# Kernel optimization log

Hardware: AMD Instinct MI355X
Metric: run time of the kernel (lower is better)

## Reference

```python
import jax, jax.numpy as jnp
import numpy as np


def _patches3x3(x):
    # x: [B,H,W,C] -> [B,H,W,9,C], SAME zero padding, patch index k = i*3+j
    B, H, W, C = x.shape
    p = jnp.pad(x, ((0, 0), (1, 1), (1, 1), (0, 0)))
    return jnp.stack([p[:, i:i + H, j:j + W, :] for i in range(3) for j in range(3)], axis=3)


def setup_inputs() -> dict:
    key = jax.random.key(0)
    k1, k2, k3 = jax.random.split(key, 3)
    B, H, W, CH, NC, DIM = 4, 80, 80, 256, 22, 256
    x = jax.random.normal(k1, (B, H, W, CH), dtype=jnp.float32)
    seg_mask = jax.random.uniform(k2, (B, H, W, NC), dtype=jnp.float32)
    # he_uniform over receptive field ch*3*3
    lim = np.sqrt(6.0 / (CH * 9)).astype(np.float32)
    conv_w = jax.random.uniform(k3, (CH, 3, 3, DIM), dtype=jnp.float32, minval=-lim, maxval=lim)
    return {"x": x, "seg_mask": seg_mask, "conv_w": conv_w}


def reference(x, seg_mask, conv_w):
    B, H, W, CH = x.shape
    NC = seg_mask.shape[-1]
    DIM = conv_w.shape[-1]
    # patches of segmentation map: [B,H,W,9,NC]
    s_patch = _patches3x3(seg_mask)
    m = seg_mask[:, :, :, None, :]                       # [B,H,W,1,NC]
    s_max = jnp.max(m, axis=-1, keepdims=True)           # [B,H,W,1,1]
    # keep patch values only for the argmax class at the center pixel
    sel = jnp.sum(jnp.where(m == s_max, s_patch, 0.0), axis=-1)  # [B,H,W,9]
    cnt = jnp.sum((sel != 0.0).astype(jnp.float32), axis=-1, keepdims=True)  # [B,H,W,1]
    norm = jnp.where(cnt > 0, 9.0 / jnp.maximum(cnt, 1.0), 0.0)  # divide_no_nan(9, cnt)
    # per-channel 3x3 patch extraction of features (== depthwise conv with eye(9))
    xp = _patches3x3(x)                                  # [B,H,W,9,CH]
    xp = xp * sel[..., None]                             # mask-gated patches
    w = conv_w.reshape(CH, 9, DIM)
    out = jnp.einsum('bhwkc,ckd->bhwd', xp, w) * norm    # [B,H,W,DIM]
    return out
```

## Files before the change

kernel.cpp:

```cpp
#include <hip/hip_runtime.h>
#include <hip/hip_bf16.h>
#include <cstdint>

#define B_ 4
#define H_ 80
#define W_ 80
#define CH_ 256
#define NC_ 22
#define DIM_ 256
#define NPIX (B_*H_*W_)

typedef unsigned short ushort;
typedef __attribute__((ext_vector_type(8))) short short8;
typedef __attribute__((ext_vector_type(4))) float floatx4;

static __device__ inline ushort f2bf(float v) {
    __hip_bfloat16 h = __float2bfloat16(v);
    ushort r;
    __builtin_memcpy(&r, &h, 2);
    return r;
}
static __device__ inline unsigned pk2(float a, float b) {
    return (unsigned)f2bf(a) | ((unsigned)f2bf(b) << 16);
}

static __device__ inline void gll16(const ushort* g, ushort* l) {
    __builtin_amdgcn_global_load_lds(
        (const __attribute__((address_space(1))) unsigned int*)g,
        (__attribute__((address_space(3))) unsigned int*)l, 16, 0, 0);
}

__global__ __launch_bounds__(256) void prep(const float* __restrict__ cw,
                                            const float* __restrict__ x,
                                            ushort* __restrict__ wbT,
                                            ushort* __restrict__ xb)
{
    __shared__ ushort ls[32][260];
    if (blockIdx.x >= 72) {
        const int bid = blockIdx.x - 72;
        const size_t idx = ((size_t)bid * 256 + threadIdx.x) * 8;
        const float4* s = (const float4*)(x + idx);
        float4 a = s[0], b = s[1];
        *(uint4*)(xb + idx) = make_uint4(pk2(a.x, a.y), pk2(a.z, a.w),
                                         pk2(b.x, b.y), pk2(b.z, b.w));
        if (bid == 0 && threadIdx.x < 64)
            *(uint4*)(xb + (size_t)NPIX * CH_ + threadIdx.x * 8) = make_uint4(0, 0, 0, 0);
        return;
    }
    const int k  = blockIdx.x / 8;
    const int c0 = (blockIdx.x % 8) * 32;
    const int c   = threadIdx.x >> 3;
    const int sg  = threadIdx.x & 7;

    const float* src = cw + ((size_t)(c0 + c) * 9 + k) * DIM_ + sg * 32;
    #pragma unroll
    for (int e = 0; e < 32; e += 4) {
        float4 v = *(const float4*)(src + e);
        unsigned* dst = (unsigned*)&ls[c][sg * 32 + e];
        dst[0] = pk2(v.x, v.y);
        dst[1] = pk2(v.z, v.w);
    }
    __syncthreads();

    const int d = threadIdx.x;
    ushort tmp[32];
    #pragma unroll
    for (int cc = 0; cc < 32; ++cc) tmp[cc] = ls[cc][d];
    uint4 o[4];
    __builtin_memcpy(o, tmp, 64);
    uint4* dst = (uint4*)(wbT + ((size_t)k * 256 + d) * 256 + c0);
    dst[0] = o[0]; dst[1] = o[1]; dst[2] = o[2]; dst[3] = o[3];
}

__global__ __launch_bounds__(256, 3) void conv3(const ushort* __restrict__ xb,
                                                const float* __restrict__ seg,
                                                const ushort* __restrict__ wbT,
                                                float* __restrict__ out)
{
    __shared__ ushort xs[2][84 * 128];
    __shared__ float  sl[9][80];

    const int tid  = threadIdx.x;
    const int lane = tid & 63;
    const int wv   = tid >> 6;
    const int ln   = lane & 15;
    const int quad = lane >> 4;
    const int d0   = blockIdx.x * 128;
    const int rt   = blockIdx.y;
    const int b    = rt / H_;
    const int h    = rt % H_;
    const ushort* zpad = xb + (size_t)NPIX * CH_;

    const int rho0 = lane >> 4;
    const int cp   = lane & 15;
    auto stage = [&](int p, int buf) {
        const int i  = p >> 1;
        const int cc = (p & 1) * 128;
        const int r  = h + i - 1;
        const bool rowok = (r >= 0) && (r < H_);
        for (int g = wv; g < 21; g += 4) {
            const int rho = g * 4 + rho0;
            const int scn = (cp & 8) | ((cp ^ rho) & 7);
            const int col = rho - 1;
            const bool v = rowok && (col >= 0) && (col < W_);
            const ushort* src = v ? (xb + (((size_t)(b * H_ + r)) * W_ + col) * CH_
                                        + cc + scn * 8)
                                  : zpad;
            gll16(src, &xs[buf][g * 512]);
        }
    };

    stage(0, 0);

    if (tid < W_) {
        const int m = tid;
        const float2* c2 = (const float2*)(seg + ((size_t)(b * H_ + h) * W_ + m) * NC_);
        float cv[NC_];
        #pragma unroll
        for (int c = 0; c < NC_ / 2; ++c) { float2 v = c2[c]; cv[2*c] = v.x; cv[2*c+1] = v.y; }
        float mx = -1e30f;
        #pragma unroll
        for (int c = 0; c < NC_; ++c) mx = fmaxf(mx, cv[c]);
        float sel[9];
        int cnt = 0;
        #pragma unroll
        for (int k = 0; k < 9; ++k) {
            int i = k / 3, j = k % 3;
            int hh = h + i - 1, ww = m + j - 1;
            float s = 0.f;
            if (hh >= 0 && hh < H_ && ww >= 0 && ww < W_) {
                const float2* n2 = (const float2*)(seg + ((size_t)(b * H_ + hh) * W_ + ww) * NC_);
                #pragma unroll
                for (int c = 0; c < NC_ / 2; ++c) {
                    float2 v = n2[c];
                    s += (cv[2*c]   == mx) ? v.x : 0.f;
                    s += (cv[2*c+1] == mx) ? v.y : 0.f;
                }
            }
            sel[k] = s;
            cnt += (s != 0.f) ? 1 : 0;
        }
        float norm = (cnt > 0) ? 9.f / (float)cnt : 0.f;
        #pragma unroll
        for (int k = 0; k < 9; ++k) sl[k][m] = sel[k] * norm;
    }

    floatx4 O[5][2];
    #pragma unroll
    for (int im = 0; im < 5; ++im)
        #pragma unroll
        for (int jn = 0; jn < 2; ++jn)
            O[im][jn] = (floatx4){0.f, 0.f, 0.f, 0.f};

    __syncthreads();

    for (int p = 0; p < 6; ++p) {
        const int buf = p & 1;
        const int i   = p >> 1;
        const int cc  = (p & 1) * 128;
        if (p < 5) stage(p + 1, buf ^ 1);

        #pragma unroll
        for (int j = 0; j < 3; ++j) {
            const int k = 3 * i + j;

            short8 Breg[8];
            #pragma unroll
            for (int kk = 0; kk < 4; ++kk)
                #pragma unroll
                for (int jn = 0; jn < 2; ++jn)
                    Breg[kk * 2 + jn] = *(const short8*)(wbT
                        + ((size_t)k * 256 + d0 + wv * 32 + jn * 16 + ln) * 256
                        + cc + kk * 32 + quad * 8);

            floatx4 P[5][2];
            #pragma unroll
            for (int im = 0; im < 5; ++im)
                #pragma unroll
                for (int jn = 0; jn < 2; ++jn)
                    P[im][jn] = (floatx4){0.f, 0.f, 0.f, 0.f};

            #pragma unroll
            for (int kk = 0; kk < 4; ++kk) {
                short8 a[5];
                #pragma unroll
                for (int im = 0; im < 5; ++im) {
                    const int rho = im * 16 + ln + j;
                    const int Gc  = 4 * kk + quad;
                    const int ch  = (Gc & 8) | ((Gc ^ rho) & 7);
                    a[im] = *(const short8*)&xs[buf][rho * 128 + ch * 8];
                }
                #pragma unroll
                for (int im = 0; im < 5; ++im)
                    #pragma unroll
                    for (int jn = 0; jn < 2; ++jn)
                        P[im][jn] = __builtin_amdgcn_mfma_f32_16x16x32_bf16(
                            a[im], Breg[kk * 2 + jn], P[im][jn], 0, 0, 0);
            }

            #pragma unroll
            for (int im = 0; im < 5; ++im) {
                const floatx4 sv = *(const floatx4*)&sl[k][im * 16 + quad * 4];
                #pragma unroll
                for (int jn = 0; jn < 2; ++jn) {
                    O[im][jn][0] += sv[0] * P[im][jn][0];
                    O[im][jn][1] += sv[1] * P[im][jn][1];
                    O[im][jn][2] += sv[2] * P[im][jn][2];
                    O[im][jn][3] += sv[3] * P[im][jn][3];
                }
            }
        }
        __syncthreads();
    }

    #pragma unroll
    for (int im = 0; im < 5; ++im) {
        #pragma unroll
        for (int jn = 0; jn < 2; ++jn) {
            const int dd = d0 + wv * 32 + jn * 16 + ln;
            #pragma unroll
            for (int r = 0; r < 4; ++r) {
                const int m = im * 16 + quad * 4 + r;
                out[((size_t)(rt * W_ + m)) * DIM_ + dd] = O[im][jn][r];
            }
        }
    }
}

extern "C" void kernel_launch(void* const* d_in, const int* in_sizes, int n_in,
                              void* d_out, int out_size, void* d_ws, size_t ws_size,
                              hipStream_t stream)
{
    const float* x   = (const float*)d_in[0];
    const float* seg = (const float*)d_in[1];
    const float* cw  = (const float*)d_in[2];
    float* out = (float*)d_out;

    ushort* wbT = (ushort*)d_ws;
    ushort* xb  = (ushort*)((char*)d_ws + 1179648);

    prep<<<dim3(72 + NPIX * CH_ / (256 * 8)), dim3(256), 0, stream>>>(cw, x, wbT, xb);
    conv3<<<dim3(2, B_ * H_), dim3(256), 0, stream>>>(xb, seg, wbT, out);
}
```

Baseline: 177.9 us.

## Fuse fp32-to-bf16 conversion of x into conv kernel staging

```diff
diff --git a/kernel.cpp b/kernel.cpp
--- a/kernel.cpp
+++ b/kernel.cpp
@@ -24,33 +24,14 @@
     return (unsigned)f2bf(a) | ((unsigned)f2bf(b) << 16);
 }
 
-static __device__ inline void gll16(const ushort* g, ushort* l) {
-    __builtin_amdgcn_global_load_lds(
-        (const __attribute__((address_space(1))) unsigned int*)g,
-        (__attribute__((address_space(3))) unsigned int*)l, 16, 0, 0);
-}
-
 __global__ __launch_bounds__(256) void prep(const float* __restrict__ cw,
-                                            const float* __restrict__ x,
-                                            ushort* __restrict__ wbT,
-                                            ushort* __restrict__ xb)
+                                            ushort* __restrict__ wbT)
 {
     __shared__ ushort ls[32][260];
-    if (blockIdx.x >= 72) {
-        const int bid = blockIdx.x - 72;
-        const size_t idx = ((size_t)bid * 256 + threadIdx.x) * 8;
-        const float4* s = (const float4*)(x + idx);
-        float4 a = s[0], b = s[1];
-        *(uint4*)(xb + idx) = make_uint4(pk2(a.x, a.y), pk2(a.z, a.w),
-                                         pk2(b.x, b.y), pk2(b.z, b.w));
-        if (bid == 0 && threadIdx.x < 64)
-            *(uint4*)(xb + (size_t)NPIX * CH_ + threadIdx.x * 8) = make_uint4(0, 0, 0, 0);
-        return;
-    }
     const int k  = blockIdx.x / 8;
     const int c0 = (blockIdx.x % 8) * 32;
-    const int c   = threadIdx.x >> 3;
-    const int sg  = threadIdx.x & 7;
+    const int c  = threadIdx.x >> 3;
+    const int sg = threadIdx.x & 7;
 
     const float* src = cw + ((size_t)(c0 + c) * 9 + k) * DIM_ + sg * 32;
     #pragma unroll
@@ -72,7 +53,7 @@
     dst[0] = o[0]; dst[1] = o[1]; dst[2] = o[2]; dst[3] = o[3];
 }
 
-__global__ __launch_bounds__(256, 3) void conv3(const ushort* __restrict__ xb,
+__global__ __launch_bounds__(256, 3) void conv4(const float* __restrict__ x,
                                                 const float* __restrict__ seg,
                                                 const ushort* __restrict__ wbT,
                                                 float* __restrict__ out)
@@ -89,28 +70,51 @@
     const int rt   = blockIdx.y;
     const int b    = rt / H_;
     const int h    = rt % H_;
-    const ushort* zpad = xb + (size_t)NPIX * CH_;
-
-    const int rho0 = lane >> 4;
-    const int cp   = lane & 15;
-    auto stage = [&](int p, int buf) {
+
+    float4 fa[2], fb[2];
+    bool   okc[2];
+
+    auto sload = [&](int p, int r0) {
         const int i  = p >> 1;
         const int cc = (p & 1) * 128;
-        const int r  = h + i - 1;
-        const bool rowok = (r >= 0) && (r < H_);
-        for (int g = wv; g < 21; g += 4) {
-            const int rho = g * 4 + rho0;
-            const int scn = (cp & 8) | ((cp ^ rho) & 7);
-            const int col = rho - 1;
-            const bool v = rowok && (col >= 0) && (col < W_);
-            const ushort* src = v ? (xb + (((size_t)(b * H_ + r)) * W_ + col) * CH_
-                                        + cc + scn * 8)
-                                  : zpad;
-            gll16(src, &xs[buf][g * 512]);
+        const int rr = h + i - 1;
+        const bool rowok = (rr >= 0) && (rr < H_);
+        #pragma unroll
+        for (int t = 0; t < 2; ++t) {
+            const int q   = tid + 256 * (r0 + t);
+            const int row = q >> 4;
+            const int cb  = q & 15;
+            const int col = row - 1;
+            const bool v = (q < 1344) && rowok && (col >= 0) && (col < W_);
+            okc[t] = v;
+            if (v) {
+                const int ch2 = (cb & 8) | ((cb ^ row) & 7);
+                const float* f = x + (((size_t)(b * H_ + rr)) * W_ + col) * CH_
+                                   + cc + ch2 * 8;
+                fa[t] = *(const float4*)f;
+                fb[t] = *(const float4*)(f + 4);
+            }
         }
     };
-
-    stage(0, 0);
+    auto sstore = [&](int buf, int r0) {
+        #pragma unroll
+        for (int t = 0; t < 2; ++t) {
+            const int q = tid + 256 * (r0 + t);
+            if (q < 1344) {
+                const int row = q >> 4;
+                const int cb  = q & 15;
+                uint4 v = okc[t]
+                    ? make_uint4(pk2(fa[t].x, fa[t].y), pk2(fa[t].z, fa[t].w),
+                                 pk2(fb[t].x, fb[t].y), pk2(fb[t].z, fb[t].w))
+                    : make_uint4(0u, 0u, 0u, 0u);
+                *(uint4*)&xs[buf][row * 128 + cb * 8] = v;
+            }
+        }
+    };
+
+    sload(0, 0); sstore(0, 0);
+    sload(0, 2); sstore(0, 2);
+    sload(0, 4); sstore(0, 4);
 
     if (tid < W_) {
         const int m = tid;
@@ -158,7 +162,6 @@
         const int buf = p & 1;
         const int i   = p >> 1;
         const int cc  = (p & 1) * 128;
-        if (p < 5) stage(p + 1, buf ^ 1);
 
         #pragma unroll
         for (int j = 0; j < 3; ++j) {
@@ -172,6 +175,8 @@
                     Breg[kk * 2 + jn] = *(const short8*)(wbT
                         + ((size_t)k * 256 + d0 + wv * 32 + jn * 16 + ln) * 256
                         + cc + kk * 32 + quad * 8);
+
+            if (p < 5) sload(p + 1, 2 * j);
 
             floatx4 P[5][2];
             #pragma unroll
@@ -197,6 +202,8 @@
                         P[im][jn] = __builtin_amdgcn_mfma_f32_16x16x32_bf16(
                             a[im], Breg[kk * 2 + jn], P[im][jn], 0, 0, 0);
             }
+
+            if (p < 5) sstore(buf ^ 1, 2 * j);
 
             #pragma unroll
             for (int im = 0; im < 5; ++im) {
@@ -237,8 +244,7 @@
     float* out = (float*)d_out;
 
     ushort* wbT = (ushort*)d_ws;
-    ushort* xb  = (ushort*)((char*)d_ws + 1179648);
-
-    prep<<<dim3(72 + NPIX * CH_ / (256 * 8)), dim3(256), 0, stream>>>(cw, x, wbT, xb);
-    conv3<<<dim3(2, B_ * H_), dim3(256), 0, stream>>>(xb, seg, wbT, out);
-}
+
+    prep<<<dim3(72), dim3(256), 0, stream>>>(cw, wbT);
+    conv4<<<dim3(2, B_ * H_), dim3(256), 0, stream>>>(x, seg, wbT, out);
+}
```

Result: slower. 327.7 us (+84.1%).
